# Kernel tuning notes

Hardware: AMD Instinct MI355X
Metric: run time of the kernel (lower is better)

## Reference

```python
import jax, jax.numpy as jnp
import numpy as np

N = 50000      # nodes
E = 800000     # edges (avg degree 16)
D = 64         # input features
H = 128        # hidden channels
C = 10         # classes
G = 500        # graphs in batch


def setup_inputs() -> dict:
    key = jax.random.key(0)
    ks = jax.random.split(key, 13)
    s = lambda f: 1.0 / np.sqrt(f)
    return {
        "x": jax.random.normal(ks[0], (N, D), jnp.float32),
        "edge_index": jax.random.randint(ks[1], (2, E), 0, N, dtype=jnp.int64),
        "batch": jnp.sort(jax.random.randint(ks[2], (N,), 0, G, dtype=jnp.int64)),
        # MLP embedder (Linear(D,D) -> ReLU -> Linear(D,D) -> ReLU)
        "emb_w1": jax.random.normal(ks[3], (D, D), jnp.float32) * s(D),
        "emb_b1": jnp.zeros((D,), jnp.float32),
        "emb_w2": jax.random.normal(ks[4], (D, D), jnp.float32) * s(D),
        "emb_b2": jnp.zeros((D,), jnp.float32),
        # 3-layer GCN: D->H, H->H, H->C
        "w1": jax.random.normal(ks[5], (D, H), jnp.float32) * s(D),
        "b1": jnp.zeros((H,), jnp.float32),
        "w2": jax.random.normal(ks[6], (H, H), jnp.float32) * s(H),
        "b2": jnp.zeros((H,), jnp.float32),
        "w3": jax.random.normal(ks[7], (H, C), jnp.float32) * s(H),
        "b3": jnp.zeros((C,), jnp.float32),
    }


def _gcn_structure(edge_index):
    # add self-loops; symmetric normalization (PyG gcn_norm)
    loop = jnp.arange(N, dtype=edge_index.dtype)
    src = jnp.concatenate([edge_index[0], loop])  # [E+N]
    dst = jnp.concatenate([edge_index[1], loop])  # [E+N]
    deg = jax.ops.segment_sum(jnp.ones_like(src, jnp.float32), dst, num_segments=N)
    dinv = jnp.where(deg > 0, jax.lax.rsqrt(deg), 0.0)
    norm = dinv[src] * dinv[dst]                  # [E+N]
    return src, dst, norm


def _gcn_conv(h, src, dst, norm, w, b):
    # X W first (cheap when out_dim small), then normalized scatter-add over edges
    hw = h @ w                                    # [N, out]
    msg = hw[src] * norm[:, None]                 # [E+N, out]
    return jax.ops.segment_sum(msg, dst, num_segments=N) + b


def reference(x, edge_index, batch, emb_w1, emb_b1, emb_w2, emb_b2,
              w1, b1, w2, b2, w3, b3):
    src, dst, norm = _gcn_structure(edge_index)
    # MLP embedder
    h = jax.nn.relu(x @ emb_w1 + emb_b1)
    h = jax.nn.relu(h @ emb_w2 + emb_b2)
    # GCN stack (ReLU between layers, none after last)
    h = jax.nn.relu(_gcn_conv(h, src, dst, norm, w1, b1))
    h = jax.nn.relu(_gcn_conv(h, src, dst, norm, w2, b2))
    h = _gcn_conv(h, src, dst, norm, w3, b3)      # [N, C]
    # scatter-mean pooling per graph
    summed = jax.ops.segment_sum(h, batch, num_segments=G)           # [G, C]
    cnt = jax.ops.segment_sum(jnp.ones((N,), jnp.float32), batch, num_segments=G)
    pooled = summed / jnp.maximum(cnt, 1.0)[:, None]
    return jax.nn.log_softmax(pooled, axis=1)
```

## Files before the change

kernel.cpp:

```cpp
#include <hip/hip_runtime.h>
#include <math.h>

#define NN 50000
#define NG 500
#define CC 10
#define NRANGE 8
#define RSIZE 6250
#define CAP 64

static inline int cdiv(int a, int b) { return (a + b - 1) / b; }

__device__ inline unsigned bf16rne(float f) {
    unsigned u = __float_as_uint(f);
    return (u + 0x7fffu + ((u >> 16) & 1u)) >> 16;
}
__device__ inline unsigned pack2bf(float a, float b) {
    return bf16rne(a) | (bf16rne(b) << 16);
}

typedef __attribute__((ext_vector_type(8))) short bf16x8;
typedef __attribute__((ext_vector_type(4))) float f32x4;

__global__ void prep_all_kernel(const float* __restrict__ w1, const float* __restrict__ w2,
                                const float* __restrict__ w3,
                                const float* __restrict__ ew1, const float* __restrict__ ew2,
                                unsigned short* __restrict__ wt1, unsigned short* __restrict__ wt2,
                                unsigned short* __restrict__ wt3,
                                unsigned short* __restrict__ ewt1, unsigned short* __restrict__ ewt2,
                                int* __restrict__ fill) {
    int i = blockIdx.x * 256 + threadIdx.x;
    if (i < NN) fill[i] = 0;
    if (i < 128 * 64) {
        int o = i / 64, k = i % 64;
        wt1[i] = (unsigned short)bf16rne(w1[k * 128 + o]);
    }
    int j = i - 128 * 64;
    if (j >= 0 && j < 128 * 128) {
        int o = j / 128, k = j % 128;
        wt2[j] = (unsigned short)bf16rne(w2[k * 128 + o]);
    }
    int m = j - 128 * 128;
    if (m >= 0 && m < 16 * 128) {
        int o = m / 128, k = m % 128;
        wt3[m] = (o < 10) ? (unsigned short)bf16rne(w3[k * 10 + o]) : 0;
    }
    int p = m - 16 * 128;
    if (p >= 0 && p < 64 * 64) {
        int o = p / 64, k = p % 64;
        ewt1[p] = (unsigned short)bf16rne(ew1[k * 64 + o]);
    }
    int q = p - 64 * 64;
    if (q >= 0 && q < 64 * 64) {
        int o = q / 64, k = q % 64;
        ewt2[q] = (unsigned short)bf16rne(ew2[k * 64 + o]);
    }
}

__global__ void bucket_fill_kernel(const int* __restrict__ src, const int* __restrict__ dst,
                                   int* __restrict__ fill, int* __restrict__ csr, int nedges) {
    int r = blockIdx.x & (NRANGE - 1);
    int q = (blockIdx.x >> 3) * 256 + threadIdx.x;
    int base = q * 4;
    if (base >= nedges) return;
    if (base + 3 < nedges) {
        int4 d = *reinterpret_cast<const int4*>(dst + base);
        int4 s = *reinterpret_cast<const int4*>(src + base);
        if (d.x / RSIZE == r) { int p = atomicAdd(&fill[d.x], 1); if (p < CAP) csr[(size_t)d.x * CAP + p] = s.x; }
        if (d.y / RSIZE == r) { int p = atomicAdd(&fill[d.y], 1); if (p < CAP) csr[(size_t)d.y * CAP + p] = s.y; }
        if (d.z / RSIZE == r) { int p = atomicAdd(&fill[d.z], 1); if (p < CAP) csr[(size_t)d.z * CAP + p] = s.z; }
        if (d.w / RSIZE == r) { int p = atomicAdd(&fill[d.w], 1); if (p < CAP) csr[(size_t)d.w * CAP + p] = s.w; }
    } else {
        for (int j = 0; j < nedges - base; ++j) {
            int d = dst[base + j];
            if (d / RSIZE == r) { int p = atomicAdd(&fill[d], 1); if (p < CAP) csr[(size_t)d * CAP + p] = src[base + j]; }
        }
    }
}

__global__ __launch_bounds__(256) void emb_mfma_kernel(
    const float* __restrict__ x,
    const unsigned short* __restrict__ ewt1, const float* __restrict__ b1e,
    const unsigned short* __restrict__ ewt2, const float* __restrict__ b2e,
    const int* __restrict__ fill, float* __restrict__ dinv,
    unsigned short* __restrict__ out )
{
    constexpr int AST = 72;
    __shared__ unsigned short sX[64][AST];
    __shared__ unsigned short sW1[64][AST];
    __shared__ unsigned short sW2[64][AST];
    __shared__ unsigned short sH[64][AST];
    __shared__ float sDv[64];
    int tid = threadIdx.x;
    int wave = tid >> 6, lane = tid & 63;
    int base = blockIdx.x * 64;
    int r0 = wave * 16;

    if (tid < 64) {
        int gn = base + tid;
        float dv = 0.f;
        if (gn < NN) {
            int c = fill[gn]; if (c > CAP) c = CAP;
            dv = rsqrtf((float)c + 1.0f);
            dinv[gn] = dv;
        }
        sDv[tid] = dv;
    }
    for (int i = tid; i < 64 * 8; i += 256) {
        int r = i >> 3, p = i & 7;
        *reinterpret_cast<uint4*>(&sW1[r][p * 8]) =
            *reinterpret_cast<const uint4*>(ewt1 + r * 64 + p * 8);
        *reinterpret_cast<uint4*>(&sW2[r][p * 8]) =
            *reinterpret_cast<const uint4*>(ewt2 + r * 64 + p * 8);
    }
    for (int i = tid; i < 64 * 16; i += 256) {
        int r = i >> 4, p = i & 15;
        int gn = base + r;
        float4 v = make_float4(0.f, 0.f, 0.f, 0.f);
        if (gn < NN) v = *reinterpret_cast<const float4*>(&x[(size_t)gn * 64 + p * 4]);
        uint2 w; w.x = pack2bf(v.x, v.y); w.y = pack2bf(v.z, v.w);
        *reinterpret_cast<uint2*>(&sX[r][p * 4]) = w;
    }
    __syncthreads();

    int colq = lane & 15;
    int rowq = (lane >> 4) * 4;
    {
        f32x4 acc[4] = {};
        #pragma unroll
        for (int ks = 0; ks < 2; ++ks) {
            bf16x8 af = *reinterpret_cast<const bf16x8*>(&sX[r0 + (lane & 15)][ks * 32 + (lane >> 4) * 8]);
            #pragma unroll
            for (int ct = 0; ct < 4; ++ct) {
                bf16x8 bfv = *reinterpret_cast<const bf16x8*>(&sW1[ct * 16 + (lane & 15)][ks * 32 + (lane >> 4) * 8]);
                acc[ct] = __builtin_amdgcn_mfma_f32_16x16x32_bf16(af, bfv, acc[ct], 0, 0, 0);
            }
        }
        #pragma unroll
        for (int ct = 0; ct < 4; ++ct) {
            int col = ct * 16 + colq;
            float bv = b1e[col];
            #pragma unroll
            for (int r = 0; r < 4; ++r)
                sH[r0 + rowq + r][col] = (unsigned short)bf16rne(fmaxf(acc[ct][r] + bv, 0.f));
        }
    }
    __syncthreads();
    {
        f32x4 acc[4] = {};
        #pragma unroll
        for (int ks = 0; ks < 2; ++ks) {
            bf16x8 af = *reinterpret_cast<const bf16x8*>(&sH[r0 + (lane & 15)][ks * 32 + (lane >> 4) * 8]);
            #pragma unroll
            for (int ct = 0; ct < 4; ++ct) {
                bf16x8 bfv = *reinterpret_cast<const bf16x8*>(&sW2[ct * 16 + (lane & 15)][ks * 32 + (lane >> 4) * 8]);
                acc[ct] = __builtin_amdgcn_mfma_f32_16x16x32_bf16(af, bfv, acc[ct], 0, 0, 0);
            }
        }
        #pragma unroll
        for (int ct = 0; ct < 4; ++ct) {
            int col = ct * 16 + colq;
            float bv = b2e[col];
            #pragma unroll
            for (int r = 0; r < 4; ++r) {
                int row = base + r0 + rowq + r;
                if (row >= NN) continue;
                float dv = sDv[r0 + rowq + r];
                out[(size_t)row * 64 + col] =
                    (unsigned short)bf16rne(fmaxf(acc[ct][r] + bv, 0.f) * dv);
            }
        }
    }
}

template <int K, int OUT, bool BIAS, bool RELU_OUT, bool SCALE_DINV, bool OUT_BF16>
__global__ __launch_bounds__(256) void mfma_mm_kernel(
    const unsigned short* __restrict__ a,
    const unsigned short* __restrict__ wt,
    const float* __restrict__ bias,
    const float* __restrict__ dinv,
    void* __restrict__ outv, int ostride)
{
    constexpr int KC = 64;
    constexpr int NCH = K / KC;
    constexpr int AST = KC + 8;
    constexpr int NCT = OUT / 16;
    __shared__ unsigned short sA[64][AST];
    __shared__ unsigned short sW[OUT][AST];
    int tid = threadIdx.x;
    int wave = tid >> 6, lane = tid & 63;
    int base = blockIdx.x * 64;
    int r0 = wave * 16;

    f32x4 acc[NCT] = {};

    for (int ch = 0; ch < NCH; ++ch) {
        if (ch) __syncthreads();
        for (int i = tid; i < 64 * 8; i += 256) {
            int r = i >> 3, p = i & 7;
            int gn = base + r;
            uint4 v = make_uint4(0, 0, 0, 0);
            if (gn < NN) v = *reinterpret_cast<const uint4*>(a + (size_t)gn * K + ch * KC + p * 8);
            *reinterpret_cast<uint4*>(&sA[r][p * 8]) = v;
        }
        for (int i = tid; i < OUT * 8; i += 256) {
            int o = i >> 3, p = i & 7;
            uint4 v = *reinterpret_cast<const uint4*>(wt + (size_t)o * K + ch * KC + p * 8);
            *reinterpret_cast<uint4*>(&sW[o][p * 8]) = v;
        }
        __syncthreads();
        #pragma unroll
        for (int ks = 0; ks < KC / 32; ++ks) {
            bf16x8 af = *reinterpret_cast<const bf16x8*>(&sA[r0 + (lane & 15)][ks * 32 + (lane >> 4) * 8]);
            #pragma unroll
            for (int ct = 0; ct < NCT; ++ct) {
                bf16x8 bfv = *reinterpret_cast<const bf16x8*>(&sW[ct * 16 + (lane & 15)][ks * 32 + (lane >> 4) * 8]);
                acc[ct] = __builtin_amdgcn_mfma_f32_16x16x32_bf16(af, bfv, acc[ct], 0, 0, 0);
            }
        }
    }

    int colq = lane & 15;
    int rowq = (lane >> 4) * 4;
    float dv[4];
    #pragma unroll
    for (int r = 0; r < 4; ++r) {
        int row = base + r0 + rowq + r;
        dv[r] = (SCALE_DINV && row < NN) ? dinv[row] : 1.0f;
    }
    #pragma unroll
    for (int ct = 0; ct < NCT; ++ct) {
        int col = ct * 16 + colq;
        float bv = BIAS ? bias[col] : 0.0f;
        #pragma unroll
        for (int r = 0; r < 4; ++r) {
            int row = base + r0 + rowq + r;
            if (row >= NN) continue;
            float v = acc[ct][r] + bv;
            if (RELU_OUT) v = fmaxf(v, 0.0f);
            if (SCALE_DINV) v *= dv[r];
            if (OUT_BF16)
                reinterpret_cast<unsigned short*>(outv)[(size_t)row * ostride + col] =
                    (unsigned short)bf16rne(v);
            else
                reinterpret_cast<float*>(outv)[(size_t)row * ostride + col] = v;
        }
    }
}

#define GACC(P) ax += __uint_as_float((P) << 16); ay += __uint_as_float((P) & 0xffff0000u)

__global__ __launch_bounds__(256) void gcn_gather64_bf16_kernel(
    const int* __restrict__ csr, const int* __restrict__ fill,
    const float* __restrict__ dinv, const unsigned* __restrict__ hw, unsigned* __restrict__ out)
{
    int tid = threadIdx.x;
    int n = blockIdx.x * 8 + (tid >> 5);
    if (n >= NN) return;
    int lane = tid & 31;
    unsigned p0 = hw[(size_t)n * 32 + lane];
    float ax = __uint_as_float(p0 << 16);
    float ay = __uint_as_float(p0 & 0xffff0000u);
    size_t s0 = (size_t)n * CAP;
    int c = fill[n]; if (c > CAP) c = CAP;
    int i = 0;
    for (; i + 7 < c; i += 8) {
        unsigned q0 = hw[(size_t)csr[s0 + i + 0] * 32 + lane];
        unsigned q1 = hw[(size_t)csr[s0 + i + 1] * 32 + lane];
        unsigned q2 = hw[(size_t)csr[s0 + i + 2] * 32 + lane];
        unsigned q3 = hw[(size_t)csr[s0 + i + 3] * 32 + lane];
        unsigned q4 = hw[(size_t)csr[s0 + i + 4] * 32 + lane];
        unsigned q5 = hw[(size_t)csr[s0 + i + 5] * 32 + lane];
        unsigned q6 = hw[(size_t)csr[s0 + i + 6] * 32 + lane];
        unsigned q7 = hw[(size_t)csr[s0 + i + 7] * 32 + lane];
        GACC(q0); GACC(q1); GACC(q2); GACC(q3);
        GACC(q4); GACC(q5); GACC(q6); GACC(q7);
    }
    for (; i + 3 < c; i += 4) {
        unsigned q0 = hw[(size_t)csr[s0 + i + 0] * 32 + lane];
        unsigned q1 = hw[(size_t)csr[s0 + i + 1] * 32 + lane];
        unsigned q2 = hw[(size_t)csr[s0 + i + 2] * 32 + lane];
        unsigned q3 = hw[(size_t)csr[s0 + i + 3] * 32 + lane];
        GACC(q0); GACC(q1); GACC(q2); GACC(q3);
    }
    for (; i < c; ++i) {
        unsigned q0 = hw[(size_t)csr[s0 + i] * 32 + lane];
        GACC(q0);
    }
    float di = dinv[n];
    out[(size_t)n * 32 + lane] = pack2bf(ax * di, ay * di);
}

__global__ __launch_bounds__(256) void gcn_gather128_bf16_kernel(
    const int* __restrict__ csr, const int* __restrict__ fill,
    const float* __restrict__ dinv, const unsigned* __restrict__ hw, const float* __restrict__ b,
    unsigned* __restrict__ out)
{
    int tid = threadIdx.x;
    int n = blockIdx.x * 4 + (tid >> 6);
    if (n >= NN) return;
    int lane = tid & 63;
    unsigned p0 = hw[(size_t)n * 64 + lane];
    float ax = __uint_as_float(p0 << 16);
    float ay = __uint_as_float(p0 & 0xffff0000u);
    size_t s0 = (size_t)n * CAP;
    int c = fill[n]; if (c > CAP) c = CAP;
    int i = 0;
    for (; i + 7 < c; i += 8) {
        unsigned q0 = hw[(size_t)csr[s0 + i + 0] * 64 + lane];
        unsigned q1 = hw[(size_t)csr[s0 + i + 1] * 64 + lane];
        unsigned q2 = hw[(size_t)csr[s0 + i + 2] * 64 + lane];
        unsigned q3 = hw[(size_t)csr[s0 + i + 3] * 64 + lane];
        unsigned q4 = hw[(size_t)csr[s0 + i + 4] * 64 + lane];
        unsigned q5 = hw[(size_t)csr[s0 + i + 5] * 64 + lane];
        unsigned q6 = hw[(size_t)csr[s0 + i + 6] * 64 + lane];
        unsigned q7 = hw[(size_t)csr[s0 + i + 7] * 64 + lane];
        GACC(q0); GACC(q1); GACC(q2); GACC(q3);
        GACC(q4); GACC(q5); GACC(q6); GACC(q7);
    }
    for (; i + 3 < c; i += 4) {
        unsigned q0 = hw[(size_t)csr[s0 + i + 0] * 64 + lane];
        unsigned q1 = hw[(size_t)csr[s0 + i + 1] * 64 + lane];
        unsigned q2 = hw[(size_t)csr[s0 + i + 2] * 64 + lane];
        unsigned q3 = hw[(size_t)csr[s0 + i + 3] * 64 + lane];
        GACC(q0); GACC(q1); GACC(q2); GACC(q3);
    }
    for (; i < c; ++i) {
        unsigned q0 = hw[(size_t)csr[s0 + i] * 64 + lane];
        GACC(q0);
    }
    float di = dinv[n];
    float2 bb = *reinterpret_cast<const float2*>(b + lane * 2);
    out[(size_t)n * 64 + lane] = pack2bf(fmaxf(bb.x + ax * di, 0.f), fmaxf(bb.y + ay * di, 0.f));
}

__global__ void gcn_gather10_kernel(
    const int* __restrict__ csr, const int* __restrict__ fill,
    const float* __restrict__ dinv, const float* __restrict__ hw, const float* __restrict__ b,
    float* __restrict__ out)
{
    int idx = blockIdx.x * 256 + threadIdx.x;
    int n = idx >> 4;
    int ch = idx & 15;
    if (n >= NN || ch >= 10) return;
    float acc = hw[n * 16 + ch];
    size_t s0 = (size_t)n * CAP;
    int c = fill[n]; if (c > CAP) c = CAP;
    int i = 0;
    for (; i + 3 < c; i += 4) {
        float a0 = hw[csr[s0 + i + 0] * 16 + ch];
        float a1 = hw[csr[s0 + i + 1] * 16 + ch];
        float a2 = hw[csr[s0 + i + 2] * 16 + ch];
        float a3 = hw[csr[s0 + i + 3] * 16 + ch];
        acc += a0 + a1 + a2 + a3;
    }
    for (; i < c; ++i)
        acc += hw[csr[s0 + i] * 16 + ch];
    out[n * 16 + ch] = b[ch] + acc * dinv[n];
}

__global__ __launch_bounds__(256) void pool_ls_kernel(
    const float* __restrict__ h3, const int* __restrict__ batch, float* __restrict__ out)
{
    __shared__ int seg[2];
    __shared__ float red[16][17];
    int g = blockIdx.x;
    int t = threadIdx.x;
    if (t < 2) {
        int target = g + t;
        int lo = 0, hi = NN;
        while (lo < hi) {
            int mid = (lo + hi) >> 1;
            if (batch[mid] < target) lo = mid + 1; else hi = mid;
        }
        seg[t] = lo;
    }
    __syncthreads();
    int s = seg[0], e = seg[1];
    int ch = t & 15, nl = t >> 4;
    float acc = 0.0f;
    for (int n = s + nl; n < e; n += 16)
        if (ch < 10) acc += h3[(size_t)n * 16 + ch];
    red[nl][ch] = acc;
    __syncthreads();
    if (t < 16) {
        float ssum = 0.0f;
        #pragma unroll
        for (int i = 0; i < 16; ++i) ssum += red[i][t];
        red[0][t] = ssum;
    }
    __syncthreads();
    if (t == 0) {
        float c = fmaxf((float)(e - s), 1.0f);
        float v[10], m = -1e30f;
        #pragma unroll
        for (int i = 0; i < 10; ++i) { v[i] = red[0][i] / c; m = fmaxf(m, v[i]); }
        float ssum = 0.0f;
        #pragma unroll
        for (int i = 0; i < 10; ++i) ssum += expf(v[i] - m);
        float lse = m + logf(ssum);
        #pragma unroll
        for (int i = 0; i < 10; ++i) out[g * 10 + i] = v[i] - lse;
    }
}

extern "C" void kernel_launch(void* const* d_in, const int* in_sizes, int n_in,
                              void* d_out, int out_size, void* d_ws, size_t ws_size,
                              hipStream_t stream)
{
    const float* x      = (const float*)d_in[0];
    const int*   ei     = (const int*)d_in[1];
    const int*   batch  = (const int*)d_in[2];
    const float* emb_w1 = (const float*)d_in[3];
    const float* emb_b1 = (const float*)d_in[4];
    const float* emb_w2 = (const float*)d_in[5];
    const float* emb_b2 = (const float*)d_in[6];
    const float* w1     = (const float*)d_in[7];
    const float* b1     = (const float*)d_in[8];
    const float* w2     = (const float*)d_in[9];
    const float* b2     = (const float*)d_in[10];
    const float* w3     = (const float*)d_in[11];
    const float* b3     = (const float*)d_in[12];

    int E = in_sizes[1] / 2;
    const int* src = ei;
    const int* dst = ei + E;

    char* ws = (char*)d_ws;
    size_t off = 0;
    unsigned short* H1b  = (unsigned short*)(ws + off); off += (size_t)NN * 128 * 2;
    unsigned short* HWB  = (unsigned short*)(ws + off); off += (size_t)NN * 128 * 2;
    unsigned short* EMB  = (unsigned short*)(ws + off); off += (size_t)NN * 64 * 2;
    unsigned short* A64g = (unsigned short*)(ws + off); off += (size_t)NN * 64 * 2;
    unsigned short* wt1  = (unsigned short*)(ws + off); off += 128 * 64 * 2;
    unsigned short* wt2  = (unsigned short*)(ws + off); off += 128 * 128 * 2;
    unsigned short* wt3  = (unsigned short*)(ws + off); off += 16 * 128 * 2;
    unsigned short* ewt1 = (unsigned short*)(ws + off); off += 64 * 64 * 2;
    unsigned short* ewt2 = (unsigned short*)(ws + off); off += 64 * 64 * 2;
    float* dinv = (float*)(ws + off); off += (size_t)NN * 4;
    int*   fill = (int*)(ws + off);   off += (size_t)NN * 4;
    int*   csr  = (int*)(ws + off);   off += (size_t)NN * CAP * 4;

    float* M3  = (float*)EMB;
    float* G10 = (float*)A64g;

    int mmgrid = cdiv(NN, 64);
    int egrid4 = cdiv(cdiv(E, 4), 256) * NRANGE;

    prep_all_kernel<<<cdiv(NN, 256), 256, 0, stream>>>(
        w1, w2, w3, emb_w1, emb_w2, wt1, wt2, wt3, ewt1, ewt2, fill);
    bucket_fill_kernel<<<egrid4, 256, 0, stream>>>(src, dst, fill, csr, E);

    emb_mfma_kernel<<<mmgrid, 256, 0, stream>>>(x, ewt1, emb_b1, ewt2, emb_b2, fill, dinv, EMB);

    gcn_gather64_bf16_kernel<<<cdiv(NN, 8), 256, 0, stream>>>(csr, fill, dinv, (unsigned*)EMB, (unsigned*)A64g);
    mfma_mm_kernel<64, 128, true, true, false, true><<<mmgrid, 256, 0, stream>>>(
        A64g, wt1, b1, nullptr, H1b, 128);

    mfma_mm_kernel<128, 128, false, false, true, true><<<mmgrid, 256, 0, stream>>>(
        H1b, wt2, nullptr, dinv, HWB, 128);
    gcn_gather128_bf16_kernel<<<cdiv(NN, 4), 256, 0, stream>>>(csr, fill, dinv, (unsigned*)HWB, b2, (unsigned*)H1b);

    mfma_mm_kernel<128, 16, false, false, true, false><<<mmgrid, 256, 0, stream>>>(
        H1b, wt3, nullptr, dinv, M3, 16);
    gcn_gather10_kernel<<<cdiv(NN * 16, 256), 256, 0, stream>>>(csr, fill, dinv, M3, b3, G10);

    pool_ls_kernel<<<NG, 256, 0, stream>>>(G10, batch, (float*)d_out);
}
```

Before: 161.9 us.

## Fuse final 10-channel gather into pooling kernel and grid-stride bucket fill

The last GCN gather (10 channels) is folded into the per-graph pooling kernel, so each graph block gathers its nodes' neighbours directly and accumulates the pooled sum. This drops one kernel launch and the G10 intermediate write and read. The edge bucketing kernel now runs on a fixed grid of 256 blocks per range with a grid-stride loop instead of one quad per thread. The cost is that pooling now runs on only 500 blocks doing the heavy gather with uneven per-graph work, which may reduce parallelism. Channels 10-15 are now also gathered, wasting some lanes.

After: 173.6 us. 7.2% more time.

```diff
diff --git a/kernel.cpp b/kernel.cpp
--- a/kernel.cpp
+++ b/kernel.cpp
@@ -7,6 +7,7 @@
 #define NRANGE 8
 #define RSIZE 6250
 #define CAP 64
+#define FILLNB 256
 
 static inline int cdiv(int a, int b) { return (a + b - 1) / b; }
 
@@ -56,23 +57,27 @@
     }
 }
 
-__global__ void bucket_fill_kernel(const int* __restrict__ src, const int* __restrict__ dst,
-                                   int* __restrict__ fill, int* __restrict__ csr, int nedges) {
+__global__ __launch_bounds__(256) void bucket_fill_kernel(
+    const int* __restrict__ src, const int* __restrict__ dst,
+    int* __restrict__ fill, int* __restrict__ csr, int nedges)
+{
     int r = blockIdx.x & (NRANGE - 1);
-    int q = (blockIdx.x >> 3) * 256 + threadIdx.x;
-    int base = q * 4;
-    if (base >= nedges) return;
-    if (base + 3 < nedges) {
-        int4 d = *reinterpret_cast<const int4*>(dst + base);
-        int4 s = *reinterpret_cast<const int4*>(src + base);
-        if (d.x / RSIZE == r) { int p = atomicAdd(&fill[d.x], 1); if (p < CAP) csr[(size_t)d.x * CAP + p] = s.x; }
-        if (d.y / RSIZE == r) { int p = atomicAdd(&fill[d.y], 1); if (p < CAP) csr[(size_t)d.y * CAP + p] = s.y; }
-        if (d.z / RSIZE == r) { int p = atomicAdd(&fill[d.z], 1); if (p < CAP) csr[(size_t)d.z * CAP + p] = s.z; }
-        if (d.w / RSIZE == r) { int p = atomicAdd(&fill[d.w], 1); if (p < CAP) csr[(size_t)d.w * CAP + p] = s.w; }
-    } else {
-        for (int j = 0; j < nedges - base; ++j) {
-            int d = dst[base + j];
-            if (d / RSIZE == r) { int p = atomicAdd(&fill[d], 1); if (p < CAP) csr[(size_t)d * CAP + p] = src[base + j]; }
+    int cb = blockIdx.x >> 3;
+    int nquads = (nedges + 3) >> 2;
+    for (int q = cb * 256 + threadIdx.x; q < nquads; q += FILLNB * 256) {
+        int base = q * 4;
+        if (base + 3 < nedges) {
+            int4 d = *reinterpret_cast<const int4*>(dst + base);
+            int4 s = *reinterpret_cast<const int4*>(src + base);
+            if (d.x / RSIZE == r) { int p = atomicAdd(&fill[d.x], 1); if (p < CAP) csr[(size_t)d.x * CAP + p] = s.x; }
+            if (d.y / RSIZE == r) { int p = atomicAdd(&fill[d.y], 1); if (p < CAP) csr[(size_t)d.y * CAP + p] = s.y; }
+            if (d.z / RSIZE == r) { int p = atomicAdd(&fill[d.z], 1); if (p < CAP) csr[(size_t)d.z * CAP + p] = s.z; }
+            if (d.w / RSIZE == r) { int p = atomicAdd(&fill[d.w], 1); if (p < CAP) csr[(size_t)d.w * CAP + p] = s.w; }
+        } else {
+            for (int j = 0; j < nedges - base; ++j) {
+                int d = dst[base + j];
+                if (d / RSIZE == r) { int p = atomicAdd(&fill[d], 1); if (p < CAP) csr[(size_t)d * CAP + p] = src[base + j]; }
+            }
         }
     }
 }
@@ -333,33 +338,10 @@
     out[(size_t)n * 64 + lane] = pack2bf(fmaxf(bb.x + ax * di, 0.f), fmaxf(bb.y + ay * di, 0.f));
 }
 
-__global__ void gcn_gather10_kernel(
+__global__ __launch_bounds__(256) void pool_g10_kernel(
     const int* __restrict__ csr, const int* __restrict__ fill,
-    const float* __restrict__ dinv, const float* __restrict__ hw, const float* __restrict__ b,
-    float* __restrict__ out)
-{
-    int idx = blockIdx.x * 256 + threadIdx.x;
-    int n = idx >> 4;
-    int ch = idx & 15;
-    if (n >= NN || ch >= 10) return;
-    float acc = hw[n * 16 + ch];
-    size_t s0 = (size_t)n * CAP;
-    int c = fill[n]; if (c > CAP) c = CAP;
-    int i = 0;
-    for (; i + 3 < c; i += 4) {
-        float a0 = hw[csr[s0 + i + 0] * 16 + ch];
-        float a1 = hw[csr[s0 + i + 1] * 16 + ch];
-        float a2 = hw[csr[s0 + i + 2] * 16 + ch];
-        float a3 = hw[csr[s0 + i + 3] * 16 + ch];
-        acc += a0 + a1 + a2 + a3;
-    }
-    for (; i < c; ++i)
-        acc += hw[csr[s0 + i] * 16 + ch];
-    out[n * 16 + ch] = b[ch] + acc * dinv[n];
-}
-
-__global__ __launch_bounds__(256) void pool_ls_kernel(
-    const float* __restrict__ h3, const int* __restrict__ batch, float* __restrict__ out)
+    const float* __restrict__ dinv, const float* __restrict__ m3, const float* __restrict__ b3,
+    const int* __restrict__ batch, float* __restrict__ out)
 {
     __shared__ int seg[2];
     __shared__ float red[16][17];
@@ -377,9 +359,24 @@
     __syncthreads();
     int s = seg[0], e = seg[1];
     int ch = t & 15, nl = t >> 4;
+    float bch = (ch < 10) ? b3[ch] : 0.0f;
     float acc = 0.0f;
-    for (int n = s + nl; n < e; n += 16)
-        if (ch < 10) acc += h3[(size_t)n * 16 + ch];
+    for (int n = s + nl; n < e; n += 16) {
+        float v = m3[(size_t)n * 16 + ch];
+        size_t s0 = (size_t)n * CAP;
+        int c = fill[n]; if (c > CAP) c = CAP;
+        int i = 0;
+        for (; i + 3 < c; i += 4) {
+            float a0 = m3[(size_t)csr[s0 + i + 0] * 16 + ch];
+            float a1 = m3[(size_t)csr[s0 + i + 1] * 16 + ch];
+            float a2 = m3[(size_t)csr[s0 + i + 2] * 16 + ch];
+            float a3 = m3[(size_t)csr[s0 + i + 3] * 16 + ch];
+            v += a0 + a1 + a2 + a3;
+        }
+        for (; i < c; ++i)
+            v += m3[(size_t)csr[s0 + i] * 16 + ch];
+        acc += bch + v * dinv[n];
+    }
     red[nl][ch] = acc;
     __syncthreads();
     if (t < 16) {
@@ -440,15 +437,13 @@
     int*   fill = (int*)(ws + off);   off += (size_t)NN * 4;
     int*   csr  = (int*)(ws + off);   off += (size_t)NN * CAP * 4;
 
-    float* M3  = (float*)EMB;
-    float* G10 = (float*)A64g;
+    float* M3 = (float*)EMB;
 
     int mmgrid = cdiv(NN, 64);
-    int egrid4 = cdiv(cdiv(E, 4), 256) * NRANGE;
 
     prep_all_kernel<<<cdiv(NN, 256), 256, 0, stream>>>(
         w1, w2, w3, emb_w1, emb_w2, wt1, wt2, wt3, ewt1, ewt2, fill);
-    bucket_fill_kernel<<<egrid4, 256, 0, stream>>>(src, dst, fill, csr, E);
+    bucket_fill_kernel<<<NRANGE * FILLNB, 256, 0, stream>>>(src, dst, fill, csr, E);
 
     emb_mfma_kernel<<<mmgrid, 256, 0, stream>>>(x, ewt1, emb_b1, ewt2, emb_b2, fill, dinv, EMB);
 
@@ -462,7 +457,6 @@
 
     mfma_mm_kernel<128, 16, false, false, true, false><<<mmgrid, 256, 0, stream>>>(
         H1b, wt3, nullptr, dinv, M3, 16);
-    gcn_gather10_kernel<<<cdiv(NN * 16, 256), 256, 0, stream>>>(csr, fill, dinv, M3, b3, G10);
-
-    pool_ls_kernel<<<NG, 256, 0, stream>>>(G10, batch, (float*)d_out);
-}
+
+    pool_g10_kernel<<<NG, 256, 0, stream>>>(csr, fill, dinv, M3, b3, batch, (float*)d_out);
+}
```
